# Performance work log

Measured on AMD Instinct MI355X. Metric: run time of the kernel, lower is better.

## Reference

```python
import jax, jax.numpy as jnp
import numpy as np

LANE_WEIGHT = 1.0   # _LANE_LOSS_WEIGHT
TEMP = 0.1          # args.score_temp

B, L, K, T = 256, 16, 64, 50
NL, NT = B * L, B * L * K


def _seg_ids(starts, n):
    # contiguous segments covering [0, n): segment id = (# starts <= i) - 1
    return (jnp.cumsum(jnp.zeros((n,), jnp.int32).at[starts].add(1)) - 1).astype(jnp.int32)


def _seg_log_softmax(x, seg, nseg):
    m = jax.ops.segment_max(x, seg, num_segments=nseg)
    z = x - m[seg]
    lse = jnp.log(jax.ops.segment_sum(jnp.exp(z), seg, num_segments=nseg))
    return z - lse[seg]


def _seg_softmax(x, seg, nseg):
    m = jax.ops.segment_max(x, seg, num_segments=nseg)
    e = jnp.exp(x - m[seg])
    s = jax.ops.segment_sum(e, seg, num_segments=nseg)
    return e / s[seg]


def setup_inputs() -> dict:
    key = jax.random.key(0)
    k1, k2, k3, k4, k5 = jax.random.split(key, 5)
    lane_scores = jax.random.normal(k1, (NL,), jnp.float32)
    traj_scores = jax.random.normal(k2, (NT, 1), jnp.float32)
    pred_candidates = jax.random.normal(k3, (NT, T, 2), jnp.float32)
    pred_gt = jax.random.normal(k4, (B, T, 2), jnp.float32)
    scales = jnp.ones((B,), jnp.float32)
    # ragged segment boundaries (here uniform, but reference only uses starts)
    cls_start_end_idx = jnp.stack([jnp.arange(B, dtype=jnp.int32) * L,
                                   jnp.arange(B, dtype=jnp.int32) * L + L], axis=1)
    trajs_start_end_idx = jnp.stack([jnp.arange(NL, dtype=jnp.int32) * K,
                                     jnp.arange(NL, dtype=jnp.int32) * K + K], axis=1)
    cls_oracle = jax.random.bernoulli(k5, 0.3, (NL,))
    # guarantee >= 1 oracle lane per sample (original divides by len(traj_loss))
    cls_oracle = cls_oracle.at[jnp.arange(B) * L].set(True)
    return {
        "lane_scores": lane_scores,
        "traj_scores": traj_scores,
        "pred_candidates": pred_candidates,
        "pred_gt": pred_gt,
        "scales": scales,
        "cls_oracle": cls_oracle,
        "cls_start_end_idx": cls_start_end_idx,
        "trajs_start_end_idx": trajs_start_end_idx,
    }


def reference(lane_scores, traj_scores, pred_candidates, pred_gt, scales,
              cls_oracle, cls_start_end_idx, trajs_start_end_idx):
    nl, nt = lane_scores.shape[0], traj_scores.shape[0]
    b = cls_start_end_idx.shape[0]
    lane_sample = _seg_ids(cls_start_end_idx[:, 0], nl)   # [NL] -> sample id
    traj_lane = _seg_ids(trajs_start_end_idx[:, 0], nt)   # [NT] -> lane id
    traj_sample = lane_sample[traj_lane]                  # [NT] -> sample id

    # ---- lane-level cross entropy per sample ----
    oracle_f = cls_oracle.astype(lane_scores.dtype)
    oracle_per_sample = jax.ops.segment_sum(oracle_f, lane_sample, num_segments=b)
    lane_target = oracle_f / oracle_per_sample[lane_sample]
    lane_logp = _seg_log_softmax(lane_scores, lane_sample, b)
    lane_loss = jax.ops.segment_sum(-lane_target * lane_logp, lane_sample,
                                    num_segments=b) * LANE_WEIGHT  # [B]

    # ---- trajectory-level cross entropy per oracle lane ----
    # ScoreEvaluator.scoring_trajs: ADE distance to GT, scale-normalized, negated
    diff = pred_candidates - pred_gt[traj_sample]          # [NT, T, 2]
    ade = jnp.mean(jnp.sqrt(jnp.sum(diff * diff, axis=-1) + 1e-12), axis=-1)
    scores = -ade / scales[traj_sample]                    # [NT]

    target = _seg_softmax(scores / TEMP, traj_lane, nl)    # softmax(scores/temp)
    out_logp = _seg_log_softmax(traj_scores[:, 0], traj_lane, nl)
    ce_per_lane = jax.ops.segment_sum(-target * out_logp, traj_lane,
                                      num_segments=nl)     # [NL]
    # only oracle lanes contribute; average over oracle-lane count per sample
    traj_loss = jax.ops.segment_sum(ce_per_lane * oracle_f, lane_sample,
                                    num_segments=b) / oracle_per_sample  # [B]

    return jnp.mean(lane_loss + traj_loss)
```

## Files before the change

kernel.cpp:

```cpp
#include <hip/hip_runtime.h>
#include <math.h>


#define LANE_WEIGHT 1.0f
#define TEMP_INV    10.0f

__global__ __launch_bounds__(256) void traj_ce_kernel(
    const float* __restrict__ pred_candidates,
    const float* __restrict__ pred_gt,
    const float* __restrict__ traj_scores,
    const float* __restrict__ scales,
    const int*   __restrict__ cls_se,
    const int*   __restrict__ trajs_se,
    float*       __restrict__ ws_ce,
    int B, int T, int NL)
{
    const int wid     = threadIdx.x >> 6;
    const int lane_id = threadIdx.x & 63;
    const int lane    = blockIdx.x * 4 + wid;
    if (lane >= NL) return;

    const int t0 = trajs_se[2 * lane];
    const int Kl = trajs_se[2 * lane + 1] - t0;

    int lo = 0, hi = B - 1;
    while (lo < hi) {
        int mid = (lo + hi + 1) >> 1;
        if (cls_se[2 * mid] <= lane) lo = mid; else hi = mid - 1;
    }
    const int sample = lo;

    const bool valid = (lane_id < Kl);
    const int  traj  = t0 + (valid ? lane_id : (Kl > 0 ? Kl - 1 : 0));

    const float4* __restrict__ tp =
        (const float4*)(pred_candidates + (size_t)traj * (T * 2));
    const float4* __restrict__ gp =
        (const float4*)(pred_gt + (size_t)sample * (T * 2));

    const int nf4 = (T * 2) / 4;
    float sum = 0.0f;
    #pragma unroll 5
    for (int r = 0; r < nf4; ++r) {
        float4 c = tp[r];
        float4 g = gp[r];
        float dx0 = c.x - g.x, dy0 = c.y - g.y;
        float dx1 = c.z - g.z, dy1 = c.w - g.w;
        sum += sqrtf(dx0 * dx0 + dy0 * dy0 + 1e-12f)
             + sqrtf(dx1 * dx1 + dy1 * dy1 + 1e-12f);
    }
    if ((T & 1) != 0) {
        const float2* tp2 = (const float2*)tp;
        const float2* gp2 = (const float2*)gp;
        float2 c = tp2[2 * nf4], g = gp2[2 * nf4];
        float dx = c.x - g.x, dy = c.y - g.y;
        sum += sqrtf(dx * dx + dy * dy + 1e-12f);
    }

    const float inv_scale = 1.0f / scales[sample];
    float sc = valid ? (-(sum / (float)T) * inv_scale * TEMP_INV) : -INFINITY;
    float m = sc;
    for (int off = 32; off; off >>= 1) m = fmaxf(m, __shfl_xor(m, off));
    float e = valid ? expf(sc - m) : 0.0f;
    float Z = e;
    for (int off = 32; off; off >>= 1) Z += __shfl_xor(Z, off);
    float target = e / Z;

    float tsc = valid ? traj_scores[traj] : -INFINITY;
    float m2 = tsc;
    for (int off = 32; off; off >>= 1) m2 = fmaxf(m2, __shfl_xor(m2, off));
    float e2 = valid ? expf(tsc - m2) : 0.0f;
    float Z2 = e2;
    for (int off = 32; off; off >>= 1) Z2 += __shfl_xor(Z2, off);
    float logp = (tsc - m2) - logf(Z2);

    float ce = valid ? (-target * logp) : 0.0f;
    for (int off = 32; off; off >>= 1) ce += __shfl_xor(ce, off);
    if (lane_id == 0) ws_ce[lane] = ce;
}

__global__ __launch_bounds__(256) void sample_loss_kernel(
    const float* __restrict__ lane_scores,
    const int*   __restrict__ cls_oracle,
    const int*   __restrict__ cls_se,
    const float* __restrict__ ws_ce,
    float*       __restrict__ out,
    int B)
{
    const int tid = threadIdx.x;
    float total = 0.0f;
    for (int s = tid; s < B; s += blockDim.x) {
        const int cs = cls_se[2 * s], cend = cls_se[2 * s + 1];
        float m = -INFINITY;
        for (int l = cs; l < cend; ++l) m = fmaxf(m, lane_scores[l]);
        float Z = 0.0f; int cnt = 0;
        for (int l = cs; l < cend; ++l) {
            Z += expf(lane_scores[l] - m);
            cnt += (cls_oracle[l] != 0);
        }
        const float lse = m + logf(Z);
        const float inv_cnt = 1.0f / (float)cnt;
        float lane_loss = 0.0f, traj_loss = 0.0f;
        for (int l = cs; l < cend; ++l) {
            if (cls_oracle[l] != 0) {
                lane_loss += -(lane_scores[l] - lse);
                traj_loss += ws_ce[l];
            }
        }
        total += lane_loss * inv_cnt * LANE_WEIGHT + traj_loss * inv_cnt;
    }
    __shared__ float s_red[256];
    s_red[tid] = total;
    __syncthreads();
    for (int off = 128; off; off >>= 1) {
        if (tid < off) s_red[tid] += s_red[tid + off];
        __syncthreads();
    }
    if (tid == 0) out[0] = s_red[0] / (float)B;
}

extern "C" void kernel_launch(void* const* d_in, const int* in_sizes, int n_in,
                              void* d_out, int out_size, void* d_ws, size_t ws_size,
                              hipStream_t stream)
{
    const float* lane_scores     = (const float*)d_in[0];
    const float* traj_scores     = (const float*)d_in[1];
    const float* pred_candidates = (const float*)d_in[2];
    const float* pred_gt         = (const float*)d_in[3];
    const float* scales          = (const float*)d_in[4];
    const int*   cls_oracle      = (const int*)d_in[5];
    const int*   cls_se          = (const int*)d_in[6];
    const int*   trajs_se        = (const int*)d_in[7];

    const int NL = in_sizes[0];
    const int NT = in_sizes[1];
    const int B  = in_sizes[6] / 2;
    const int T  = in_sizes[2] / (NT * 2);

    float* ws_ce = (float*)d_ws;
    float* out   = (float*)d_out;

    const int nblocks = (NL + 3) / 4;
    traj_ce_kernel<<<nblocks, 256, 0, stream>>>(
        pred_candidates, pred_gt, traj_scores, scales,
        cls_se, trajs_se, ws_ce, B, T, NL);

    sample_loss_kernel<<<1, 256, 0, stream>>>(
        lane_scores, cls_oracle, cls_se, ws_ce, out, B);
}
```

Baseline: 186.7 us.

## Fuse trajectory CE and sample loss into one cooperative kernel with grid sync

Merges the per-lane trajectory cross-entropy kernel and the single-block sample reduction into one cooperative launch. A persistent grid of at most 512 blocks loops over lanes, then a grid-wide barrier lets block 0 compute the final loss. Candidate loads become nontemporal vector loads. This removes a second kernel launch, but it adds grid-sync overhead, caps parallelism at 512 blocks, and adds cooperative-launch setup cost.

```diff
diff --git a/kernel.cpp b/kernel.cpp
--- a/kernel.cpp
+++ b/kernel.cpp
@@ -1,95 +1,106 @@
 #include <hip/hip_runtime.h>
+#include <hip/hip_cooperative_groups.h>
 #include <math.h>
+
+namespace cg = cooperative_groups;
 
 
 #define LANE_WEIGHT 1.0f
 #define TEMP_INV    10.0f
 
-__global__ __launch_bounds__(256) void traj_ce_kernel(
+typedef float v4f __attribute__((ext_vector_type(4)));
+
+__device__ inline v4f nt_load_v4(const v4f* p) {
+    return __builtin_nontemporal_load(p);
+}
+
+__global__ __launch_bounds__(256) void dual_classify_coop(
     const float* __restrict__ pred_candidates,
     const float* __restrict__ pred_gt,
     const float* __restrict__ traj_scores,
     const float* __restrict__ scales,
+    const float* __restrict__ lane_scores,
+    const int*   __restrict__ cls_oracle,
     const int*   __restrict__ cls_se,
     const int*   __restrict__ trajs_se,
     float*       __restrict__ ws_ce,
+    float*       __restrict__ out,
     int B, int T, int NL)
 {
-    const int wid     = threadIdx.x >> 6;
-    const int lane_id = threadIdx.x & 63;
-    const int lane    = blockIdx.x * 4 + wid;
-    if (lane >= NL) return;
-
-    const int t0 = trajs_se[2 * lane];
-    const int Kl = trajs_se[2 * lane + 1] - t0;
-
-    int lo = 0, hi = B - 1;
-    while (lo < hi) {
-        int mid = (lo + hi + 1) >> 1;
-        if (cls_se[2 * mid] <= lane) lo = mid; else hi = mid - 1;
-    }
-    const int sample = lo;
-
-    const bool valid = (lane_id < Kl);
-    const int  traj  = t0 + (valid ? lane_id : (Kl > 0 ? Kl - 1 : 0));
-
-    const float4* __restrict__ tp =
-        (const float4*)(pred_candidates + (size_t)traj * (T * 2));
-    const float4* __restrict__ gp =
-        (const float4*)(pred_gt + (size_t)sample * (T * 2));
+    const int wid      = threadIdx.x >> 6;
+    const int lane_id  = threadIdx.x & 63;
+    const int gwave    = blockIdx.x * 4 + wid;
+    const int n_gwaves = gridDim.x * 4;
 
     const int nf4 = (T * 2) / 4;
-    float sum = 0.0f;
-    #pragma unroll 5
-    for (int r = 0; r < nf4; ++r) {
-        float4 c = tp[r];
-        float4 g = gp[r];
-        float dx0 = c.x - g.x, dy0 = c.y - g.y;
-        float dx1 = c.z - g.z, dy1 = c.w - g.w;
-        sum += sqrtf(dx0 * dx0 + dy0 * dy0 + 1e-12f)
-             + sqrtf(dx1 * dx1 + dy1 * dy1 + 1e-12f);
-    }
-    if ((T & 1) != 0) {
-        const float2* tp2 = (const float2*)tp;
-        const float2* gp2 = (const float2*)gp;
-        float2 c = tp2[2 * nf4], g = gp2[2 * nf4];
-        float dx = c.x - g.x, dy = c.y - g.y;
-        sum += sqrtf(dx * dx + dy * dy + 1e-12f);
+
+    for (int lane = gwave; lane < NL; lane += n_gwaves) {
+        const int t0 = trajs_se[2 * lane];
+        const int Kl = trajs_se[2 * lane + 1] - t0;
+
+        int lo = 0, hi = B - 1;
+        while (lo < hi) {
+            int mid = (lo + hi + 1) >> 1;
+            if (cls_se[2 * mid] <= lane) lo = mid; else hi = mid - 1;
+        }
+        const int sample = lo;
+
+        const bool valid = (lane_id < Kl);
+        const int  traj  = t0 + (valid ? lane_id : (Kl > 0 ? Kl - 1 : 0));
+
+        const v4f* __restrict__ tp =
+            (const v4f*)(pred_candidates + (size_t)traj * (T * 2));
+        const v4f* __restrict__ gp =
+            (const v4f*)(pred_gt + (size_t)sample * (T * 2));
+
+        float sum = 0.0f;
+        #pragma unroll 5
+        for (int r = 0; r < nf4; ++r) {
+            v4f c = nt_load_v4(tp + r);
+            v4f g = gp[r];
+            float dx0 = c.x - g.x, dy0 = c.y - g.y;
+            float dx1 = c.z - g.z, dy1 = c.w - g.w;
+            sum += sqrtf(dx0 * dx0 + dy0 * dy0 + 1e-12f)
+                 + sqrtf(dx1 * dx1 + dy1 * dy1 + 1e-12f);
+        }
+        if ((T & 1) != 0) {
+            const float2* tp2 = (const float2*)tp;
+            const float2* gp2 = (const float2*)gp;
+            float2 c = tp2[2 * nf4], g = gp2[2 * nf4];
+            float dx = c.x - g.x, dy = c.y - g.y;
+            sum += sqrtf(dx * dx + dy * dy + 1e-12f);
+        }
+
+        const float inv_scale = 1.0f / scales[sample];
+        float sc = valid ? (-(sum / (float)T) * inv_scale * TEMP_INV)
+                         : -INFINITY;
+        float m = sc;
+        for (int off = 32; off; off >>= 1) m = fmaxf(m, __shfl_xor(m, off));
+        float e = valid ? expf(sc - m) : 0.0f;
+        float Z = e;
+        for (int off = 32; off; off >>= 1) Z += __shfl_xor(Z, off);
+        float target = e / Z;
+
+        float tsc = valid ? traj_scores[traj] : -INFINITY;
+        float m2 = tsc;
+        for (int off = 32; off; off >>= 1) m2 = fmaxf(m2, __shfl_xor(m2, off));
+        float e2 = valid ? expf(tsc - m2) : 0.0f;
+        float Z2 = e2;
+        for (int off = 32; off; off >>= 1) Z2 += __shfl_xor(Z2, off);
+        float logp = (tsc - m2) - logf(Z2);
+
+        float ce = valid ? (-target * logp) : 0.0f;
+        for (int off = 32; off; off >>= 1) ce += __shfl_xor(ce, off);
+        if (lane_id == 0) ws_ce[lane] = ce;
     }
 
-    const float inv_scale = 1.0f / scales[sample];
-    float sc = valid ? (-(sum / (float)T) * inv_scale * TEMP_INV) : -INFINITY;
-    float m = sc;
-    for (int off = 32; off; off >>= 1) m = fmaxf(m, __shfl_xor(m, off));
-    float e = valid ? expf(sc - m) : 0.0f;
-    float Z = e;
-    for (int off = 32; off; off >>= 1) Z += __shfl_xor(Z, off);
-    float target = e / Z;
+    __threadfence();
+    cg::this_grid().sync();
 
-    float tsc = valid ? traj_scores[traj] : -INFINITY;
-    float m2 = tsc;
-    for (int off = 32; off; off >>= 1) m2 = fmaxf(m2, __shfl_xor(m2, off));
-    float e2 = valid ? expf(tsc - m2) : 0.0f;
-    float Z2 = e2;
-    for (int off = 32; off; off >>= 1) Z2 += __shfl_xor(Z2, off);
-    float logp = (tsc - m2) - logf(Z2);
-
-    float ce = valid ? (-target * logp) : 0.0f;
-    for (int off = 32; off; off >>= 1) ce += __shfl_xor(ce, off);
-    if (lane_id == 0) ws_ce[lane] = ce;
-}
-
-__global__ __launch_bounds__(256) void sample_loss_kernel(
-    const float* __restrict__ lane_scores,
-    const int*   __restrict__ cls_oracle,
-    const int*   __restrict__ cls_se,
-    const float* __restrict__ ws_ce,
-    float*       __restrict__ out,
-    int B)
-{
+    if (blockIdx.x != 0) return;
     const int tid = threadIdx.x;
     float total = 0.0f;
-    for (int s = tid; s < B; s += blockDim.x) {
+    for (int s = tid; s < B; s += 256) {
         const int cs = cls_se[2 * s], cend = cls_se[2 * s + 1];
         float m = -INFINITY;
         for (int l = cs; l < cend; ++l) m = fmaxf(m, lane_scores[l]);
@@ -134,17 +145,21 @@
 
     const int NL = in_sizes[0];
     const int NT = in_sizes[1];
-    const int B  = in_sizes[6] / 2;
-    const int T  = in_sizes[2] / (NT * 2);
+    int B = in_sizes[6] / 2;
+    int T = in_sizes[2] / (NT * 2);
 
     float* ws_ce = (float*)d_ws;
     float* out   = (float*)d_out;
 
-    const int nblocks = (NL + 3) / 4;
-    traj_ce_kernel<<<nblocks, 256, 0, stream>>>(
-        pred_candidates, pred_gt, traj_scores, scales,
-        cls_se, trajs_se, ws_ce, B, T, NL);
+    int nblocks = (NL + 3) / 4;
+    if (nblocks > 512) nblocks = 512;
 
-    sample_loss_kernel<<<1, 256, 0, stream>>>(
-        lane_scores, cls_oracle, cls_se, ws_ce, out, B);
+    void* args[] = {
+        (void*)&pred_candidates, (void*)&pred_gt, (void*)&traj_scores,
+        (void*)&scales, (void*)&lane_scores, (void*)&cls_oracle,
+        (void*)&cls_se, (void*)&trajs_se, (void*)&ws_ce, (void*)&out,
+        (void*)&B, (void*)&T, (void*)&NL
+    };
+    hipLaunchCooperativeKernel((const void*)dual_classify_coop,
+                               dim3(nblocks), dim3(256), args, 0, stream);
 }
```

Result: slower. 380.0 us (+103.5%).
